# Performance work log

Hardware: AMD Instinct MI355X
Metric: run time of the kernel (lower is better)

## Reference

```python
import jax, jax.numpy as jnp
import numpy as np

SQ, B, NH, HD = 2048, 2, 16, 128  # seq, batch, heads, head_dim


def setup_inputs() -> dict:
    key = jax.random.key(0)
    kq, kk, kv = jax.random.split(key, 3)
    shape = (SQ, B, NH, HD)
    return {
        "query": jax.random.normal(kq, shape, dtype=jnp.float32),
        "key": jax.random.normal(kk, shape, dtype=jnp.float32),
        "value": jax.random.normal(kv, shape, dtype=jnp.float32),
        "attention_mask": jnp.ones((B, 1, SQ, SQ), dtype=bool),
    }


def reference(query, key, value, attention_mask):
    # query/key/value: [s, b, n, h]
    sq, b, n_heads, hn = query.shape
    norm_factor = jnp.sqrt(jnp.asarray(hn, query.dtype))
    # QK^T -> [b, n, sq, sk]
    scores = jnp.einsum("sbnh,tbnh->bnst", query, key) / norm_factor
    probs = jax.nn.softmax(scores, axis=-1, where=attention_mask)
    # PV -> [s, b, n, h]  (dropout is identity at p=0.0 / eval)
    context = jnp.einsum("bnst,tbnh->sbnh", probs, value)
    return context.reshape(sq, b, n_heads * hn)
```

## Files before the change

### kernel.cpp

```cpp
#include <hip/hip_runtime.h>
#include <hip/hip_bf16.h>
#include <math.h>


#define SQ 2048
#define NBH 32
#define HD 128
#define RSTRIDE 4096
#define BQ 256
#define BK 64
#define NKT (SQ / BK)
#define HELEMS (SQ * HD)
#define SCALE_LOG2E 0.12751879523499918f
#define THR_LOG2 8.0f

typedef __attribute__((ext_vector_type(4)))  float f32x4;
typedef __attribute__((ext_vector_type(16))) float f32x16;
typedef __attribute__((ext_vector_type(4)))  short s16x4;
typedef __attribute__((ext_vector_type(8)))  short s16x8;

#define MFMA32(a, b, c) __builtin_amdgcn_mfma_f32_32x32x16_bf16((a), (b), (c), 0, 0, 0)

__device__ __forceinline__ short f2bf(float f) {
    __hip_bfloat16 h = __float2bfloat16(f);
    return __builtin_bit_cast(short, h);
}
__device__ __forceinline__ unsigned pk2(float lo, float hi) {
    return (unsigned)(unsigned short)f2bf(lo) | ((unsigned)(unsigned short)f2bf(hi) << 16);
}

__device__ __forceinline__ void stage16(const void* g, void* l) {
    __builtin_amdgcn_global_load_lds(
        (const __attribute__((address_space(1))) unsigned int*)g,
        (__attribute__((address_space(3))) unsigned int*)l, 16, 0, 0);
}

__global__ __launch_bounds__(256) void prep_qk(const float* __restrict__ Q,
                                               const float* __restrict__ K,
                                               short* __restrict__ wq,
                                               short* __restrict__ wk) {
    const int id = blockIdx.x * 256 + threadIdx.x;
    const int bh = id >> 15;
    const int s  = (id >> 4) & 2047;
    const int c  = id & 15;
    const size_t outoff = (size_t)bh * HELEMS + (size_t)s * HD + c * 8;
    {
        const float* src = Q + (size_t)s * RSTRIDE + bh * HD + c * 8;
        f32x4 a = *(const f32x4*)src;
        f32x4 b = *(const f32x4*)(src + 4);
        s16x8 f;
        #pragma unroll
        for (int j = 0; j < 4; ++j) {
            f[j]     = f2bf(a[j] * SCALE_LOG2E);
            f[4 + j] = f2bf(b[j] * SCALE_LOG2E);
        }
        *(s16x8*)(wq + outoff) = f;
    }
    {
        const int cl = c ^ (s & 7);
        const float* src = K + (size_t)s * RSTRIDE + bh * HD + cl * 8;
        f32x4 a = *(const f32x4*)src;
        f32x4 b = *(const f32x4*)(src + 4);
        s16x8 f;
        #pragma unroll
        for (int j = 0; j < 4; ++j) { f[j] = f2bf(a[j]); f[4 + j] = f2bf(b[j]); }
        *(s16x8*)(wk + outoff) = f;
    }
}

__global__ __launch_bounds__(256) void prep_v(const float* __restrict__ V,
                                              short* __restrict__ wv) {
    const int kt = blockIdx.x;
    const int bh = blockIdx.y;
    const int tid = threadIdx.x;
    __shared__ short L[64 * 132];

    #pragma unroll
    for (int it = 0; it < 8; ++it) {
        const int id = it * 256 + tid;
        const int row = id >> 5, p = id & 31;
        f32x4 a = *(const f32x4*)(V + (size_t)(kt * BK + row) * RSTRIDE + bh * HD + p * 4);
        s16x4 f;
        #pragma unroll
        for (int j = 0; j < 4; ++j) f[j] = f2bf(a[j]);
        *(s16x4*)&L[row * 132 + p * 4] = f;
    }
    __syncthreads();
    #pragma unroll
    for (int it = 0; it < 4; ++it) {
        const int id = it * 256 + tid;
        const int dim = id >> 3, c = id & 7;
        const int klb = (c ^ (dim & 7)) * 8;
        s16x8 f;
        #pragma unroll
        for (int j = 0; j < 8; ++j) f[j] = L[(klb + j) * 132 + dim];
        *(s16x8*)(wv + (size_t)bh * HELEMS + (size_t)dim * SQ + kt * BK + c * 8) = f;
    }
}

__global__ __launch_bounds__(512) void fa_fwd3(const short* __restrict__ Qb,
                                               const short* __restrict__ Kb,
                                               const short* __restrict__ Vb,
                                               float* __restrict__ O) {
    const int qt   = blockIdx.x;
    const int bh   = blockIdx.y;
    const int tid  = threadIdx.x;
    const int w    = tid >> 6;
    const int lane = tid & 63;
    const int l32  = lane & 31;
    const int hi   = lane >> 5;

    __shared__ short Kt[2][BK * HD];
    __shared__ short Vt[2][HD * BK];

    const size_t hb = (size_t)bh * HELEMS;
    const int q = qt * BQ + w * 32 + l32;

    s16x8 qf[8];
    {
        const short* qp = Qb + hb + (size_t)q * HD + hi * 8;
        #pragma unroll
        for (int kd = 0; kd < 8; ++kd) qf[kd] = *(const s16x8*)(qp + kd * 16);
    }

    f32x16 acc[4];
    #pragma unroll
    for (int db = 0; db < 4; ++db)
        #pragma unroll
        for (int i = 0; i < 16; ++i) acc[db][i] = 0.0f;
    float m = -INFINITY, l = 0.0f;

    auto STAGE = [&](int kt, int buf) {
        if (w < 4) {
            const short* kg = Kb + hb + (size_t)kt * (BK * HD) + w * 2048 + lane * 8;
            short* ld = &Kt[buf][w * 2048 + lane * 8];
            #pragma unroll
            for (int j = 0; j < 4; ++j)
                stage16(kg + j * 512, ld + j * 512);
        } else {
            const int w4 = w - 4;
            #pragma unroll
            for (int j = 0; j < 4; ++j) {
                const int dim = w4 * 32 + j * 8 + (lane >> 3);
                const short* vg = Vb + hb + (size_t)dim * SQ + kt * BK + (lane & 7) * 8;
                short* ld = &Vt[buf][(w4 * 32 + j * 8) * BK + lane * 8];
                stage16(vg, ld);
            }
        }
    };

    STAGE(0, 0);
    __syncthreads();
    int buf = 0;

    for (int kt = 0; kt < NKT; ++kt) {
        if (kt + 1 < NKT) STAGE(kt + 1, buf ^ 1);

        f32x16 sc[2];
        #pragma unroll
        for (int kb = 0; kb < 2; ++kb) {
            #pragma unroll
            for (int i = 0; i < 16; ++i) sc[kb][i] = 0.0f;
            const int key = kb * 32 + l32;
            #pragma unroll
            for (int kd = 0; kd < 8; ++kd) {
                const int elem = key * HD + (((kd << 1) | hi) ^ (key & 7)) * 8;
                s16x8 kf = *(const s16x8*)&Kt[buf][elem];
                sc[kb] = MFMA32(kf, qf[kd], sc[kb]);
            }
        }

        float mt = sc[0][0];
        #pragma unroll
        for (int kb = 0; kb < 2; ++kb)
            #pragma unroll
            for (int r = 0; r < 16; ++r)
                if (kb | r) mt = fmaxf(mt, sc[kb][r]);
        const float m0 = fmaxf(mt, __shfl_xor(mt, 32, 64));
        const bool need = (m0 > m + THR_LOG2);
        const float mn = need ? fmaxf(m, m0) : m;
        if (__any(need)) {
            const float alpha = exp2f(m - mn);
            m = mn;
            l *= alpha;
            #pragma unroll
            for (int db = 0; db < 4; ++db) acc[db] *= alpha;
        }
        float ls = 0.0f;
        #pragma unroll
        for (int kb = 0; kb < 2; ++kb)
            #pragma unroll
            for (int r = 0; r < 16; ++r) {
                const float p = exp2f(sc[kb][r] - m);
                sc[kb][r] = p;
                ls += p;
            }
        l += ls;

        s16x8 pa[4];
        #pragma unroll
        for (int ks = 0; ks < 4; ++ks) {
            const int kb = ks >> 1;
            const int j  = (2 * ks) & 3, j2 = (2 * ks + 1) & 3;
            unsigned a0 = pk2(sc[kb][4 * j + 0],  sc[kb][4 * j + 1]);
            unsigned a1 = pk2(sc[kb][4 * j + 2],  sc[kb][4 * j + 3]);
            unsigned b0 = pk2(sc[kb][4 * j2 + 0], sc[kb][4 * j2 + 1]);
            unsigned b1 = pk2(sc[kb][4 * j2 + 2], sc[kb][4 * j2 + 3]);
#if __has_builtin(__builtin_amdgcn_permlane32_swap)
            auto r0 = __builtin_amdgcn_permlane32_swap(a0, b0, false, false);
            auto r1 = __builtin_amdgcn_permlane32_swap(a1, b1, false, false);
            union { unsigned u[4]; s16x8 v; } P;
            P.u[0] = r0[0]; P.u[1] = r1[0]; P.u[2] = r0[1]; P.u[3] = r1[1];
#else
            const unsigned s0 = __shfl_xor(hi ? a0 : b0, 32, 64);
            const unsigned s1 = __shfl_xor(hi ? a1 : b1, 32, 64);
            union { unsigned u[4]; s16x8 v; } P;
            P.u[0] = hi ? s0 : a0; P.u[1] = hi ? s1 : a1;
            P.u[2] = hi ? b0 : s0; P.u[3] = hi ? b1 : s1;
#endif
            pa[ks] = P.v;
        }

        #pragma unroll
        for (int db = 0; db < 4; ++db) {
            const int dim = db * 32 + l32;
            #pragma unroll
            for (int ks = 0; ks < 4; ++ks) {
                const int elem = dim * BK + ((((ks << 1) | hi) ^ (dim & 7)) << 3);
                s16x8 vf = *(const s16x8*)&Vt[buf][elem];
                acc[db] = MFMA32(vf, pa[ks], acc[db]);
            }
        }

        __syncthreads();
        buf ^= 1;
    }

    const float lf = l + __shfl_xor(l, 32, 64);
    const float invl = 1.0f / lf;
    float* op = O + (size_t)q * RSTRIDE + bh * HD;
    #pragma unroll
    for (int db = 0; db < 4; ++db)
        #pragma unroll
        for (int j = 0; j < 4; ++j) {
            f32x4 o;
            #pragma unroll
            for (int r = 0; r < 4; ++r) o[r] = acc[db][4 * j + r] * invl;
            *(f32x4*)(op + db * 32 + j * 8 + hi * 4) = o;
        }
}

__global__ __launch_bounds__(256) void fa_fwd_legacy(const float* __restrict__ Q,
                                                     const float* __restrict__ K,
                                                     const float* __restrict__ V,
                                                     float* __restrict__ O) {
    const int qt   = blockIdx.x;
    const int bh   = blockIdx.y;
    const int tid  = threadIdx.x;
    const int w    = tid >> 6;
    const int lane = tid & 63;
    const int l16  = lane & 15;
    const int lg   = lane >> 4;

    __shared__ short Kt[BK * HD];
    __shared__ short Vt[HD * BK];
    __shared__ short Pl[4][16 * 72];

    const int headoff = bh * HD;
    s16x8 qf[4];
    {
        const int qrow = qt * 64 + w * 16 + l16;
        const float* qp = Q + (size_t)qrow * RSTRIDE + headoff + lg * 8;
        #pragma unroll
        for (int ks = 0; ks < 4; ++ks) {
            f32x4 a = *(const f32x4*)(qp + ks * 32);
            f32x4 b = *(const f32x4*)(qp + ks * 32 + 4);
            s16x8 f;
            #pragma unroll
            for (int j = 0; j < 4; ++j) {
                f[j]     = f2bf(a[j] * SCALE_LOG2E);
                f[4 + j] = f2bf(b[j] * SCALE_LOG2E);
            }
            qf[ks] = f;
        }
    }
    f32x4 acc[8];
    #pragma unroll
    for (int i = 0; i < 8; ++i)
        #pragma unroll
        for (int j = 0; j < 4; ++j) acc[i][j] = 0.0f;
    float mrow[4], lrow[4];
    #pragma unroll
    for (int r = 0; r < 4; ++r) { mrow[r] = -INFINITY; lrow[r] = 0.0f; }
    const int skey = tid >> 2;
    const int sdc  = tid & 3;
    const int va   = tid >> 3;
    const int vdc  = tid & 7;

    for (int kt = 0; kt < NKT; ++kt) {
        __syncthreads();
        {
            const float* kp = K + (size_t)(kt * BK + skey) * RSTRIDE + headoff;
            #pragma unroll
            for (int c = 0; c < 4; ++c) {
                const int d0 = c * 32 + sdc * 8;
                f32x4 a = *(const f32x4*)(kp + d0);
                f32x4 b = *(const f32x4*)(kp + d0 + 4);
                s16x8 f;
                #pragma unroll
                for (int j = 0; j < 4; ++j) { f[j] = f2bf(a[j]); f[4 + j] = f2bf(b[j]); }
                const int elem = (skey * HD + d0) ^ ((skey & 7) << 3);
                *(s16x8*)&Kt[elem] = f;
            }
        }
        {
            const float* vp0 = V + (size_t)(kt * BK + va * 2) * RSTRIDE + headoff;
            const float* vp1 = vp0 + RSTRIDE;
            #pragma unroll
            for (int c = 0; c < 4; ++c) {
                const int d0 = c * 32 + vdc * 4;
                f32x4 a0 = *(const f32x4*)(vp0 + d0);
                f32x4 a1 = *(const f32x4*)(vp1 + d0);
                #pragma unroll
                for (int j = 0; j < 4; ++j) {
                    const int dim = d0 + j;
                    const int s = (dim ^ (dim >> 3)) & 7;
                    const int elem = (dim * BK + va * 2) ^ (s << 3);
                    union { short u[2]; int i; } pr;
                    pr.u[0] = f2bf(a0[j]);
                    pr.u[1] = f2bf(a1[j]);
                    *(int*)&Vt[elem] = pr.i;
                }
            }
        }
        __syncthreads();
        f32x4 sc[4];
        #pragma unroll
        for (int t = 0; t < 4; ++t) {
            #pragma unroll
            for (int j = 0; j < 4; ++j) sc[t][j] = 0.0f;
            const int key = t * 16 + l16;
            #pragma unroll
            for (int ks = 0; ks < 4; ++ks) {
                const int elem = (key * HD + ks * 32 + lg * 8) ^ ((key & 7) << 3);
                s16x8 kf = *(const s16x8*)&Kt[elem];
                sc[t] = __builtin_amdgcn_mfma_f32_16x16x32_bf16(qf[ks], kf, sc[t], 0, 0, 0);
            }
        }
        float alpha[4];
        #pragma unroll
        for (int r = 0; r < 4; ++r) {
            float m0 = fmaxf(fmaxf(sc[0][r], sc[1][r]), fmaxf(sc[2][r], sc[3][r]));
            #pragma unroll
            for (int d = 1; d < 16; d <<= 1) m0 = fmaxf(m0, __shfl_xor(m0, d, 64));
            const float mnew = fmaxf(mrow[r], m0);
            alpha[r] = exp2f(mrow[r] - mnew);
            mrow[r] = mnew;
        }
        float rsum[4] = {0.f, 0.f, 0.f, 0.f};
        #pragma unroll
        for (int t = 0; t < 4; ++t)
            #pragma unroll
            for (int r = 0; r < 4; ++r) {
                const float p = exp2f(sc[t][r] - mrow[r]);
                sc[t][r] = p;
                rsum[r] += p;
            }
        #pragma unroll
        for (int r = 0; r < 4; ++r) {
            #pragma unroll
            for (int d = 1; d < 16; d <<= 1) rsum[r] += __shfl_xor(rsum[r], d, 64);
            lrow[r] = lrow[r] * alpha[r] + rsum[r];
        }
        #pragma unroll
        for (int ct = 0; ct < 8; ++ct)
            #pragma unroll
            for (int r = 0; r < 4; ++r) acc[ct][r] *= alpha[r];
        #pragma unroll
        for (int t = 0; t < 4; ++t)
            #pragma unroll
            for (int r = 0; r < 4; ++r)
                Pl[w][(lg * 4 + r) * 72 + t * 16 + l16] = f2bf(sc[t][r]);
        s16x8 pf[2];
        #pragma unroll
        for (int ks = 0; ks < 2; ++ks)
            pf[ks] = *(const s16x8*)&Pl[w][l16 * 72 + ks * 32 + lg * 8];
        #pragma unroll
        for (int ct = 0; ct < 8; ++ct) {
            const int dim = ct * 16 + l16;
            const int s = (dim ^ (dim >> 3)) & 7;
            #pragma unroll
            for (int ks = 0; ks < 2; ++ks) {
                const int elem = (dim * BK + ks * 32 + lg * 8) ^ (s << 3);
                s16x8 vf = *(const s16x8*)&Vt[elem];
                acc[ct] = __builtin_amdgcn_mfma_f32_16x16x32_bf16(pf[ks], vf, acc[ct], 0, 0, 0);
            }
        }
    }
    float inv_l[4];
    #pragma unroll
    for (int r = 0; r < 4; ++r) inv_l[r] = 1.0f / lrow[r];
    const int orow0 = qt * 64 + w * 16;
    #pragma unroll
    for (int ct = 0; ct < 8; ++ct) {
        const int col = ct * 16 + l16;
        #pragma unroll
        for (int r = 0; r < 4; ++r) {
            const int row = orow0 + lg * 4 + r;
            O[(size_t)row * RSTRIDE + headoff + col] = acc[ct][r] * inv_l[r];
        }
    }
}

extern "C" void kernel_launch(void* const* d_in, const int* in_sizes, int n_in,
                              void* d_out, int out_size, void* d_ws, size_t ws_size,
                              hipStream_t stream) {
    const float* Q = (const float*)d_in[0];
    const float* K = (const float*)d_in[1];
    const float* V = (const float*)d_in[2];
    float* O = (float*)d_out;

    const size_t need = (size_t)3 * NBH * HELEMS * sizeof(short);
    if (ws_size >= need) {
        short* wq = (short*)d_ws;
        short* wk = wq + (size_t)NBH * HELEMS;
        short* wv = wk + (size_t)NBH * HELEMS;
        prep_qk<<<4096, 256, 0, stream>>>(Q, K, wq, wk);
        prep_v<<<dim3(NKT, NBH), 256, 0, stream>>>(V, wv);
        fa_fwd3<<<dim3(SQ / BQ, NBH), 512, 0, stream>>>(wq, wk, wv, O);
    } else {
        fa_fwd_legacy<<<dim3(SQ / 64, NBH), 256, 0, stream>>>(Q, K, V, O);
    }
}
```

Baseline: 120.5 us.

## Halve query tile, remap blocks per XCD, add setprio and packed bf16 convert

Shrinks the query tile per block from 256 to 128 rows with 256 threads, so the grid grows to 512 blocks and each wave now stages both K and V. Block IDs are remapped so blocks sharing a head land on the same XCD, which is meant to improve L2 reuse of K/V. It also wraps MFMA sections in s_setprio, splits the max and sum reductions into four independent chains, and uses v_cvt_pk_bf16_f32 inline asm for packing. The smaller tile doubles K/V staging traffic per query row, in exchange for more blocks and better occupancy.

```diff
diff --git a/kernel.cpp b/kernel.cpp
--- a/kernel.cpp
+++ b/kernel.cpp
@@ -7,7 +7,7 @@
 #define NBH 32
 #define HD 128
 #define RSTRIDE 4096
-#define BQ 256
+#define BQ 128
 #define BK 64
 #define NKT (SQ / BK)
 #define HELEMS (SQ * HD)
@@ -26,7 +26,9 @@
     return __builtin_bit_cast(short, h);
 }
 __device__ __forceinline__ unsigned pk2(float lo, float hi) {
-    return (unsigned)(unsigned short)f2bf(lo) | ((unsigned)(unsigned short)f2bf(hi) << 16);
+    unsigned r;
+    asm("v_cvt_pk_bf16_f32 %0, %1, %2" : "=v"(r) : "v"(lo), "v"(hi));
+    return r;
 }
 
 __device__ __forceinline__ void stage16(const void* g, void* l) {
@@ -98,12 +100,16 @@
     }
 }
 
-__global__ __launch_bounds__(512) void fa_fwd3(const short* __restrict__ Qb,
+__global__ __launch_bounds__(256) void fa_fwd3(const short* __restrict__ Qb,
                                                const short* __restrict__ Kb,
                                                const short* __restrict__ Vb,
                                                float* __restrict__ O) {
-    const int qt   = blockIdx.x;
-    const int bh   = blockIdx.y;
+    const int id  = blockIdx.x;
+    const int xcd = id & 7;
+    const int s8  = id >> 3;
+    const int bh  = xcd * 4 + (s8 >> 4);
+    const int qt  = s8 & 15;
+
     const int tid  = threadIdx.x;
     const int w    = tid >> 6;
     const int lane = tid & 63;
@@ -131,21 +137,16 @@
     float m = -INFINITY, l = 0.0f;
 
     auto STAGE = [&](int kt, int buf) {
-        if (w < 4) {
-            const short* kg = Kb + hb + (size_t)kt * (BK * HD) + w * 2048 + lane * 8;
-            short* ld = &Kt[buf][w * 2048 + lane * 8];
-            #pragma unroll
-            for (int j = 0; j < 4; ++j)
-                stage16(kg + j * 512, ld + j * 512);
-        } else {
-            const int w4 = w - 4;
-            #pragma unroll
-            for (int j = 0; j < 4; ++j) {
-                const int dim = w4 * 32 + j * 8 + (lane >> 3);
-                const short* vg = Vb + hb + (size_t)dim * SQ + kt * BK + (lane & 7) * 8;
-                short* ld = &Vt[buf][(w4 * 32 + j * 8) * BK + lane * 8];
-                stage16(vg, ld);
-            }
+        const short* kg = Kb + hb + (size_t)kt * (BK * HD) + w * 2048 + lane * 8;
+        short* kld = &Kt[buf][w * 2048 + lane * 8];
+        #pragma unroll
+        for (int j = 0; j < 4; ++j)
+            stage16(kg + j * 512, kld + j * 512);
+        #pragma unroll
+        for (int j = 0; j < 4; ++j) {
+            const int dim = w * 32 + j * 8 + (lane >> 3);
+            const short* vg = Vb + hb + (size_t)dim * SQ + kt * BK + (lane & 7) * 8;
+            stage16(vg, &Vt[buf][(w * 32 + j * 8) * BK + lane * 8]);
         }
     };
 
@@ -157,6 +158,7 @@
         if (kt + 1 < NKT) STAGE(kt + 1, buf ^ 1);
 
         f32x16 sc[2];
+        __builtin_amdgcn_s_setprio(1);
         #pragma unroll
         for (int kb = 0; kb < 2; ++kb) {
             #pragma unroll
@@ -169,13 +171,20 @@
                 sc[kb] = MFMA32(kf, qf[kd], sc[kb]);
             }
         }
-
-        float mt = sc[0][0];
+        __builtin_amdgcn_s_setprio(0);
+
+        float mt0 = sc[0][0], mt1 = sc[0][1], mt2 = sc[0][2], mt3 = sc[0][3];
         #pragma unroll
         for (int kb = 0; kb < 2; ++kb)
             #pragma unroll
-            for (int r = 0; r < 16; ++r)
-                if (kb | r) mt = fmaxf(mt, sc[kb][r]);
+            for (int r = 0; r < 16; r += 4) {
+                if (kb == 0 && r == 0) continue;
+                mt0 = fmaxf(mt0, sc[kb][r + 0]);
+                mt1 = fmaxf(mt1, sc[kb][r + 1]);
+                mt2 = fmaxf(mt2, sc[kb][r + 2]);
+                mt3 = fmaxf(mt3, sc[kb][r + 3]);
+            }
+        const float mt = fmaxf(fmaxf(mt0, mt1), fmaxf(mt2, mt3));
         const float m0 = fmaxf(mt, __shfl_xor(mt, 32, 64));
         const bool need = (m0 > m + THR_LOG2);
         const float mn = need ? fmaxf(m, m0) : m;
@@ -186,16 +195,20 @@
             #pragma unroll
             for (int db = 0; db < 4; ++db) acc[db] *= alpha;
         }
-        float ls = 0.0f;
+        float lsp0 = 0.f, lsp1 = 0.f, lsp2 = 0.f, lsp3 = 0.f;
         #pragma unroll
         for (int kb = 0; kb < 2; ++kb)
             #pragma unroll
-            for (int r = 0; r < 16; ++r) {
-                const float p = exp2f(sc[kb][r] - m);
-                sc[kb][r] = p;
-                ls += p;
-            }
-        l += ls;
+            for (int r = 0; r < 16; r += 4) {
+                float p0 = exp2f(sc[kb][r + 0] - m);
+                float p1 = exp2f(sc[kb][r + 1] - m);
+                float p2 = exp2f(sc[kb][r + 2] - m);
+                float p3 = exp2f(sc[kb][r + 3] - m);
+                sc[kb][r + 0] = p0; sc[kb][r + 1] = p1;
+                sc[kb][r + 2] = p2; sc[kb][r + 3] = p3;
+                lsp0 += p0; lsp1 += p1; lsp2 += p2; lsp3 += p3;
+            }
+        l += (lsp0 + lsp1) + (lsp2 + lsp3);
 
         s16x8 pa[4];
         #pragma unroll
@@ -221,6 +234,7 @@
             pa[ks] = P.v;
         }
 
+        __builtin_amdgcn_s_setprio(1);
         #pragma unroll
         for (int db = 0; db < 4; ++db) {
             const int dim = db * 32 + l32;
@@ -231,6 +245,7 @@
                 acc[db] = MFMA32(vf, pa[ks], acc[db]);
             }
         }
+        __builtin_amdgcn_s_setprio(0);
 
         __syncthreads();
         buf ^= 1;
@@ -427,7 +442,7 @@
         short* wv = wk + (size_t)NBH * HELEMS;
         prep_qk<<<4096, 256, 0, stream>>>(Q, K, wq, wk);
         prep_v<<<dim3(NKT, NBH), 256, 0, stream>>>(V, wv);
-        fa_fwd3<<<dim3(SQ / BQ, NBH), 512, 0, stream>>>(wq, wk, wv, O);
+        fa_fwd3<<<(SQ / BQ) * NBH, 256, 0, stream>>>(wq, wk, wv, O);
     } else {
         fa_fwd_legacy<<<dim3(SQ / 64, NBH), 256, 0, stream>>>(Q, K, V, O);
     }
```

Result: slower. 180.5 us (+49.8%).
